# Optimization experiments

Measured on AMD Instinct MI355X. Metric: run time of the kernel, lower is better.

## Reference

```python
import jax, jax.numpy as jnp
import numpy as np

# Mamba-1.4B-like dims
BATCH, SEQ, HID = 1, 2048, 2048
INTER, STATE, DT_RANK, KCONV = 4096, 16, 128, 4


def setup_inputs() -> dict:
    key = jax.random.key(0)
    ks = jax.random.split(key, 8)
    f = jnp.float32
    return {
        "input_states": jax.random.normal(ks[0], (BATCH, SEQ, HID), f),
        "in_proj_w": jax.random.normal(ks[1], (HID, 2 * INTER), f) * (HID ** -0.5),
        "conv_w": jax.random.normal(ks[2], (INTER, 1, KCONV), f) * (KCONV ** -0.5),  # (O, I/groups=1, K) depthwise
        "conv_b": jnp.zeros((INTER,), f),
        "x_proj_w": jax.random.normal(ks[3], (INTER, DT_RANK + 2 * STATE), f) * (INTER ** -0.5),
        "dt_proj_w": jax.random.normal(ks[4], (DT_RANK, INTER), f) * (DT_RANK ** -0.5),
        "dt_proj_b": jax.random.normal(ks[5], (INTER,), f) * 0.1,
        "A_log": jnp.log(jnp.broadcast_to(jnp.arange(1, STATE + 1, dtype=f), (INTER, STATE))),
        "D": jnp.ones((INTER,), f),
        "out_proj_w": jax.random.normal(ks[6], (INTER, HID), f) * (INTER ** -0.5),
    }


def _mamba_forward(input_states, in_proj_w, conv_w, conv_b, x_proj_w,
                   dt_proj_w, dt_proj_b, A_log, D, out_proj_w):
    Bsz, L, _ = input_states.shape
    Idim, _, K = conv_w.shape
    N = A_log.shape[1]
    R = dt_proj_w.shape[0]

    proj = input_states @ in_proj_w                       # (B, L, 2I)
    hidden, gate = jnp.split(proj, 2, axis=-1)            # each (B, L, I)

    # depthwise causal conv over sequence (pad K-1, keep first L outputs)
    xc = jnp.swapaxes(hidden, 1, 2)                       # (B, I, L)
    xc = jax.lax.conv_general_dilated(
        xc, conv_w, window_strides=(1,), padding=((K - 1, K - 1),),
        feature_group_count=Idim)
    xc = xc[:, :, :L] + conv_b[None, :, None]
    u = jax.nn.silu(jnp.swapaxes(xc, 1, 2))               # (B, L, I)

    # input-dependent SSM params
    ssm_in = u @ x_proj_w                                 # (B, L, R + 2N)
    dt_in, Bc, Cc = jnp.split(ssm_in, [R, R + N], axis=-1)
    dt = jax.nn.softplus(dt_in @ dt_proj_w + dt_proj_b)   # (B, L, I)
    A = -jnp.exp(A_log)                                   # (I, N)

    def step(state, xs):
        dt_t, B_t, C_t, u_t = xs                          # (B,I) (B,N) (B,N) (B,I)
        dA = jnp.exp(dt_t[:, :, None] * A[None])          # (B, I, N)
        state = state * dA + (dt_t * u_t)[:, :, None] * B_t[:, None, :]
        y_t = jnp.einsum('bin,bn->bi', state, C_t)
        return state, y_t

    xs = (jnp.swapaxes(dt, 0, 1), jnp.swapaxes(Bc, 0, 1),
          jnp.swapaxes(Cc, 0, 1), jnp.swapaxes(u, 0, 1))
    state0 = jnp.zeros((Bsz, Idim, N), dt.dtype)
    _, ys = jax.lax.scan(step, state0, xs)                # (L, B, I)
    y = jnp.swapaxes(ys, 0, 1)                            # (B, L, I)

    y = (y + u * D) * jax.nn.silu(gate)
    return y @ out_proj_w                                 # (B, L, H)


def reference(input_states, in_proj_w, conv_w, conv_b, x_proj_w,
              dt_proj_w, dt_proj_b, A_log, D, out_proj_w):
    return _mamba_forward(input_states, in_proj_w, conv_w, conv_b, x_proj_w,
                          dt_proj_w, dt_proj_b, A_log, D, out_proj_w)
```

## Files before the change

### kernel.cpp

```cpp
#include <hip/hip_runtime.h>
#include <stdint.h>

#define LSEQ 2048
#define HID  2048
#define IDIM 4096
#define NSTATE 16
#define RRANK 128
#define GDIM 160

#define GCHUNK 64
#define TCHUNK (LSEQ / GCHUNK)

typedef _Float16 f16x8 __attribute__((ext_vector_type(8)));
typedef float f32x4 __attribute__((ext_vector_type(4)));

#define GLOAD_LDS16(g, l) __builtin_amdgcn_global_load_lds( \
    (const __attribute__((address_space(1))) void*)(g),     \
    (__attribute__((address_space(3))) void*)(l), 16, 0, 0)

__global__ void f32_to_f16_kernel(const float* __restrict__ in, _Float16* __restrict__ out, int n) {
    int i = blockIdx.x * 256 + threadIdx.x;
    if (i < n) out[i] = (_Float16)in[i];
}

__global__ __launch_bounds__(256)
void transpose_f32_f16_kernel(const float* __restrict__ in, _Float16* __restrict__ out,
                              int R, int C) {
    __shared__ _Float16 tile[64][66];
    const int c0 = blockIdx.x * 64, r0 = blockIdx.y * 64;
    const int t = threadIdx.x;
    const int tx = t & 15, ty = t >> 4;
    const int ox = t & 7, oy = t >> 3;
    const bool full = (c0 + 64 <= C) && (r0 + 64 <= R);
    if (full) {
        #pragma unroll
        for (int j = 0; j < 4; ++j) {
            int r = ty + j * 16;
            float4 v = *(const float4*)(in + (long)(r0 + r) * C + c0 + tx * 4);
            tile[r][tx * 4 + 0] = (_Float16)v.x;
            tile[r][tx * 4 + 1] = (_Float16)v.y;
            tile[r][tx * 4 + 2] = (_Float16)v.z;
            tile[r][tx * 4 + 3] = (_Float16)v.w;
        }
        __syncthreads();
        #pragma unroll
        for (int j = 0; j < 2; ++j) {
            int c = oy + j * 32;
            f16x8 v;
            #pragma unroll
            for (int e = 0; e < 8; ++e) v[e] = tile[ox * 8 + e][c];
            *(f16x8*)(out + (long)(c0 + c) * R + r0 + ox * 8) = v;
        }
    } else {
        #pragma unroll
        for (int j = 0; j < 4; ++j) {
            int r = ty + j * 16;
            #pragma unroll
            for (int e = 0; e < 4; ++e) {
                int c = c0 + tx * 4 + e;
                float v = (r0 + r < R && c < C) ? in[(long)(r0 + r) * C + c] : 0.f;
                tile[r][tx * 4 + e] = (_Float16)v;
            }
        }
        __syncthreads();
        #pragma unroll
        for (int j = 0; j < 2; ++j) {
            int c = c0 + oy + j * 32;
            if (c < C) {
                #pragma unroll
                for (int e = 0; e < 8; ++e) {
                    int r = r0 + ox * 8 + e;
                    if (r < R) out[(long)c * R + r] = tile[ox * 8 + e][oy + j * 32];
                }
            }
        }
    }
}

#define BM 128
#define BK 64

template <typename CT, int BN_>
__global__ __launch_bounds__(256)
void gemm_bt_kernel(const _Float16* __restrict__ A, const _Float16* __restrict__ Bt,
                    CT* __restrict__ C, int M, int N, int K, int kc) {
    constexpr int NI = BN_ / 32;
    constexpr int NISS_B = BN_ * 8 / 256;
    __shared__ _Float16 As[BM * BK];
    __shared__ _Float16 Bs[BN_ * BK];
    const int m0 = blockIdx.y * BM;
    const int n0 = blockIdx.x * BN_;
    const int t = threadIdx.x;
    const int wave = t >> 6;
    const int lane = t & 63;
    const int wm = wave >> 1, wn = wave & 1;
    const int lrow = lane & 15;
    const int quad = lane >> 4;
    const int sw8 = (lrow & 7) * 8;

    f32x4 acc[4][NI];
    #pragma unroll
    for (int mi = 0; mi < 4; ++mi)
        #pragma unroll
        for (int ni = 0; ni < NI; ++ni)
            #pragma unroll
            for (int r = 0; r < 4; ++r)
                acc[mi][ni][r] = 0.f;

    const int k_begin = blockIdx.z * kc;
    const _Float16* pA[4];
    #pragma unroll
    for (int j = 0; j < 4; ++j) {
        int s = j * 256 + t;
        int row = s >> 3;
        int ch = (s & 7) ^ (row & 7);
        pA[j] = A + (long)(m0 + row) * K + ch * 8 + k_begin;
    }
    const _Float16* pB[NISS_B];
    #pragma unroll
    for (int j = 0; j < NISS_B; ++j) {
        int s = j * 256 + t;
        int row = s >> 3;
        int ch = (s & 7) ^ (row & 7);
        pB[j] = Bt + (long)(n0 + row) * K + ch * 8 + k_begin;
    }

    for (int kk = 0; kk < kc; kk += BK) {
        #pragma unroll
        for (int j = 0; j < 4; ++j) {
            GLOAD_LDS16(pA[j], As + (j * 256 + wave * 64) * 8);
            pA[j] += BK;
        }
        #pragma unroll
        for (int j = 0; j < NISS_B; ++j) {
            GLOAD_LDS16(pB[j], Bs + (j * 256 + wave * 64) * 8);
            pB[j] += BK;
        }
        __syncthreads();

        #pragma unroll
        for (int h = 0; h < 2; ++h) {
            const int qoff = (h * 32 + quad * 8) ^ sw8;
            f16x8 af[4], bf[NI];
            #pragma unroll
            for (int mi = 0; mi < 4; ++mi)
                af[mi] = *(const f16x8*)(As + (wm * 64 + mi * 16 + lrow) * BK + qoff);
            #pragma unroll
            for (int ni = 0; ni < NI; ++ni)
                bf[ni] = *(const f16x8*)(Bs + (wn * (BN_ / 2) + ni * 16 + lrow) * BK + qoff);
            #pragma unroll
            for (int mi = 0; mi < 4; ++mi)
                #pragma unroll
                for (int ni = 0; ni < NI; ++ni)
                    acc[mi][ni] = __builtin_amdgcn_mfma_f32_16x16x32_f16(af[mi], bf[ni], acc[mi][ni], 0, 0, 0);
        }
        __syncthreads();
    }

    CT* Cz = C + (long)blockIdx.z * M * N;
    #pragma unroll
    for (int mi = 0; mi < 4; ++mi) {
        #pragma unroll
        for (int ni = 0; ni < NI; ++ni) {
            int col = n0 + wn * (BN_ / 2) + ni * 16 + lrow;
            if (col < N) {
                #pragma unroll
                for (int r = 0; r < 4; ++r) {
                    int row = m0 + wm * 64 + mi * 16 + quad * 4 + r;
                    Cz[(long)row * N + col] = (CT)acc[mi][ni][r];
                }
            }
        }
    }
}

__global__ void xproj_reduce_kernel(const float* __restrict__ part, float* __restrict__ ssm,
                                    _Float16* __restrict__ dtin) {
    int idx = blockIdx.x * 256 + threadIdx.x;
    if (idx >= LSEQ * GDIM) return;
    int t = idx / GDIM;
    int c = idx - t * GDIM;
    float v = 0.f;
    #pragma unroll
    for (int k = 0; k < 8; ++k)
        v += part[((long)k * LSEQ + t) * 256 + c];
    ssm[idx] = v;
    if (c < RRANK) dtin[t * RRANK + c] = (_Float16)v;
}

__global__ void opart_reduce_kernel(const float* __restrict__ part, float* __restrict__ out) {
    int idx = blockIdx.x * 256 + threadIdx.x;
    out[idx] = part[idx] + part[idx + (long)LSEQ * HID];
}

__global__ void conv_silu_kernel(const _Float16* __restrict__ proj, const float* __restrict__ w,
                                 const float* __restrict__ b, _Float16* __restrict__ u16) {
    int idx = blockIdx.x * 256 + threadIdx.x;
    int i0 = (idx & 511) * 8;
    int t0 = (idx >> 9) * 4;
    f16x8 r[7];
    #pragma unroll
    for (int k = 0; k < 7; ++k) {
        int tt = t0 - 3 + k;
        if (tt >= 0) r[k] = *(const f16x8*)(proj + (long)tt * (2 * IDIM) + i0);
        else         r[k] = f16x8{0,0,0,0,0,0,0,0};
    }
    float4 wv[8]; float bb[8];
    #pragma unroll
    for (int j = 0; j < 8; ++j) { wv[j] = ((const float4*)w)[i0 + j]; bb[j] = b[i0 + j]; }
    #pragma unroll
    for (int tt = 0; tt < 4; ++tt) {
        f16x8 res;
        #pragma unroll
        for (int j = 0; j < 8; ++j) {
            float a = bb[j] + (float)r[tt][j] * wv[j].x + (float)r[tt+1][j] * wv[j].y
                            + (float)r[tt+2][j] * wv[j].z + (float)r[tt+3][j] * wv[j].w;
            res[j] = (_Float16)(a / (1.f + __expf(-a)));
        }
        *(f16x8*)(u16 + (long)(t0 + tt) * IDIM + i0) = res;
    }
}

__device__ __forceinline__ float softplus_f(float x) {
    if (x > 20.f) return x;
    return log1pf(__expf(x));
}
__device__ __forceinline__ float silu_f(float x) {
    return x / (1.f + __expf(-x));
}

__global__ __launch_bounds__(256)
void scan_pass1_kernel(const _Float16* __restrict__ dtlin, const float* __restrict__ dtb,
                       const float* __restrict__ ssm, const _Float16* __restrict__ u16,
                       const float* __restrict__ A_log,
                       float* __restrict__ Pc, float* __restrict__ Sc) {
    const int c = blockIdx.y;
    const int i = blockIdx.x * 256 + threadIdx.x;

    __shared__ float Bs[TCHUNK * 16];
    for (int idx = threadIdx.x; idx < TCHUNK * 16; idx += 256) {
        int t = idx >> 4, n = idx & 15;
        Bs[idx] = ssm[(c * TCHUNK + t) * GDIM + RRANK + n];
    }
    __syncthreads();

    float A[16];
    {
        const float4* Ap = (const float4*)(A_log + i * 16);
        #pragma unroll
        for (int q = 0; q < 4; ++q) {
            float4 v = Ap[q];
            A[q * 4 + 0] = -__expf(v.x);
            A[q * 4 + 1] = -__expf(v.y);
            A[q * 4 + 2] = -__expf(v.z);
            A[q * 4 + 3] = -__expf(v.w);
        }
    }
    const float dtbi = dtb[i];

    float s[16], p[16];
    #pragma unroll
    for (int n = 0; n < 16; ++n) { s[n] = 0.f; p[n] = 1.f; }

    long base = (long)c * TCHUNK * IDIM + i;
    for (int t = 0; t < TCHUNK; ++t) {
        float dt = softplus_f((float)dtlin[base + (long)t * IDIM] + dtbi);
        float dtu = dt * (float)u16[base + (long)t * IDIM];
        #pragma unroll
        for (int n = 0; n < 16; ++n) {
            float dA = __expf(dt * A[n]);
            s[n] = s[n] * dA + dtu * Bs[t * 16 + n];
            p[n] *= dA;
        }
    }

    long o = ((long)c * IDIM + i) * 16;
    #pragma unroll
    for (int q = 0; q < 4; ++q) {
        *(float4*)(Pc + o + q * 4) = make_float4(p[q*4+0], p[q*4+1], p[q*4+2], p[q*4+3]);
        *(float4*)(Sc + o + q * 4) = make_float4(s[q*4+0], s[q*4+1], s[q*4+2], s[q*4+3]);
    }
}

__global__ void scan_combine_kernel(const float* __restrict__ Pc, float* __restrict__ ScInit) {
    int tid = blockIdx.x * 256 + threadIdx.x;
    const long stride = (long)IDIM * 16;
    float p4[4], s4[4];
    #pragma unroll
    for (int k = 0; k < 4; ++k) {
        p4[k] = Pc[(long)k * stride + tid];
        s4[k] = ScInit[(long)k * stride + tid];
    }
    float carry = 0.f;
    for (int g = 0; g < GCHUNK / 4; ++g) {
        float pc[4], sc[4];
        #pragma unroll
        for (int k = 0; k < 4; ++k) { pc[k] = p4[k]; sc[k] = s4[k]; }
        if (g + 1 < GCHUNK / 4) {
            #pragma unroll
            for (int k = 0; k < 4; ++k) {
                long o2 = (long)((g + 1) * 4 + k) * stride + tid;
                p4[k] = Pc[o2];
                s4[k] = ScInit[o2];
            }
        }
        #pragma unroll
        for (int k = 0; k < 4; ++k) {
            long o = (long)(g * 4 + k) * stride + tid;
            ScInit[o] = carry;
            carry = carry * pc[k] + sc[k];
        }
    }
}

__global__ __launch_bounds__(256)
void scan_pass3_kernel(const _Float16* __restrict__ dtlin, const float* __restrict__ dtb,
                       const float* __restrict__ ssm, const _Float16* __restrict__ u16,
                       const _Float16* __restrict__ proj, const float* __restrict__ A_log,
                       const float* __restrict__ Dp, const float* __restrict__ Init,
                       _Float16* __restrict__ y16) {
    const int c = blockIdx.y;
    const int i = blockIdx.x * 256 + threadIdx.x;

    __shared__ float Bs[TCHUNK * 16];
    __shared__ float Cs[TCHUNK * 16];
    for (int idx = threadIdx.x; idx < TCHUNK * 16; idx += 256) {
        int t = idx >> 4, n = idx & 15;
        Bs[idx] = ssm[(c * TCHUNK + t) * GDIM + RRANK + n];
        Cs[idx] = ssm[(c * TCHUNK + t) * GDIM + RRANK + NSTATE + n];
    }
    __syncthreads();

    float A[16];
    {
        const float4* Ap = (const float4*)(A_log + i * 16);
        #pragma unroll
        for (int q = 0; q < 4; ++q) {
            float4 v = Ap[q];
            A[q * 4 + 0] = -__expf(v.x);
            A[q * 4 + 1] = -__expf(v.y);
            A[q * 4 + 2] = -__expf(v.z);
            A[q * 4 + 3] = -__expf(v.w);
        }
    }
    const float dtbi = dtb[i];
    const float Dv = Dp[i];

    float s[16];
    {
        long o = ((long)c * IDIM + i) * 16;
        #pragma unroll
        for (int q = 0; q < 4; ++q) {
            float4 v = *(const float4*)(Init + o + q * 4);
            s[q*4+0] = v.x; s[q*4+1] = v.y; s[q*4+2] = v.z; s[q*4+3] = v.w;
        }
    }

    long base = (long)c * TCHUNK * IDIM + i;
    for (int t = 0; t < TCHUNK; ++t) {
        float dt = softplus_f((float)dtlin[base + (long)t * IDIM] + dtbi);
        float uv = (float)u16[base + (long)t * IDIM];
        float dtu = dt * uv;
        float y = 0.f;
        #pragma unroll
        for (int n = 0; n < 16; ++n) {
            float dA = __expf(dt * A[n]);
            s[n] = s[n] * dA + dtu * Bs[t * 16 + n];
            y += s[n] * Cs[t * 16 + n];
        }
        int tg = c * TCHUNK + t;
        float g = (float)proj[(long)tg * (2 * IDIM) + IDIM + i];
        float out = (y + uv * Dv) * silu_f(g);
        y16[base + (long)t * IDIM] = (_Float16)out;
    }
}

extern "C" void kernel_launch(void* const* d_in, const int* in_sizes, int n_in,
                              void* d_out, int out_size, void* d_ws, size_t ws_size,
                              hipStream_t stream) {
    const float* x_in  = (const float*)d_in[0];
    const float* w_in  = (const float*)d_in[1];
    const float* cw    = (const float*)d_in[2];
    const float* cb    = (const float*)d_in[3];
    const float* xw    = (const float*)d_in[4];
    const float* dtw   = (const float*)d_in[5];
    const float* dtb   = (const float*)d_in[6];
    const float* alog  = (const float*)d_in[7];
    const float* Dp    = (const float*)d_in[8];
    const float* ow    = (const float*)d_in[9];
    float* out = (float*)d_out;

    char* p = (char*)d_ws;
    auto alloc = [&](size_t bytes) { char* r = p; p += (bytes + 255) & ~255ull; return r; };
    _Float16* Xf    = (_Float16*)alloc((size_t)LSEQ * HID * 2);
    _Float16* Wt1   = (_Float16*)alloc((size_t)2 * IDIM * HID * 2);
    _Float16* proj  = (_Float16*)alloc((size_t)LSEQ * 2 * IDIM * 2);
    _Float16* u16   = (_Float16*)alloc((size_t)LSEQ * IDIM * 2);
    _Float16* Wt2   = (_Float16*)alloc((size_t)256 * IDIM * 2);
    float*    ssm   = (float*)alloc((size_t)LSEQ * GDIM * 4);
    _Float16* dtin  = (_Float16*)alloc((size_t)LSEQ * RRANK * 2);
    _Float16* Wt3   = (_Float16*)alloc((size_t)IDIM * RRANK * 2);
    _Float16* dtlin = (_Float16*)alloc((size_t)LSEQ * IDIM * 2);
    _Float16* Wt4   = (_Float16*)alloc((size_t)HID * IDIM * 2);
    _Float16* y16   = (_Float16*)alloc((size_t)LSEQ * IDIM * 2);

    float* xpart = (float*)Wt1;
    float* Pc = (float*)Wt1;
    float* Sc = Pc + (size_t)GCHUNK * IDIM * 16;
    float* opart = (float*)Wt1;

    f32_to_f16_kernel<<<(LSEQ * HID) / 256, 256, 0, stream>>>(x_in, Xf, LSEQ * HID);
    transpose_f32_f16_kernel<<<dim3(2 * IDIM / 64, HID / 64), 256, 0, stream>>>(w_in, Wt1, HID, 2 * IDIM);
    transpose_f32_f16_kernel<<<dim3((GDIM + 63) / 64, IDIM / 64), 256, 0, stream>>>(xw, Wt2, IDIM, GDIM);
    transpose_f32_f16_kernel<<<dim3(IDIM / 64, RRANK / 64), 256, 0, stream>>>(dtw, Wt3, RRANK, IDIM);
    transpose_f32_f16_kernel<<<dim3(HID / 64, IDIM / 64), 256, 0, stream>>>(ow, Wt4, IDIM, HID);

    gemm_bt_kernel<_Float16, 128><<<dim3(2 * IDIM / 128, LSEQ / BM, 1), 256, 0, stream>>>(
        Xf, Wt1, proj, LSEQ, 2 * IDIM, HID, HID);
    conv_silu_kernel<<<(LSEQ / 4) * (IDIM / 8) / 256, 256, 0, stream>>>(proj, cw, cb, u16);
    gemm_bt_kernel<float, 128><<<dim3(2, LSEQ / BM, 8), 256, 0, stream>>>(
        u16, Wt2, xpart, LSEQ, 256, IDIM, IDIM / 8);
    xproj_reduce_kernel<<<(LSEQ * GDIM + 255) / 256, 256, 0, stream>>>(xpart, ssm, dtin);
    gemm_bt_kernel<_Float16, 128><<<dim3(IDIM / 128, LSEQ / BM, 1), 256, 0, stream>>>(
        dtin, Wt3, dtlin, LSEQ, IDIM, RRANK, RRANK);
    scan_pass1_kernel<<<dim3(IDIM / 256, GCHUNK), 256, 0, stream>>>(
        dtlin, dtb, ssm, u16, alog, Pc, Sc);
    scan_combine_kernel<<<(IDIM * NSTATE) / 256, 256, 0, stream>>>(Pc, Sc);
    scan_pass3_kernel<<<dim3(IDIM / 256, GCHUNK), 256, 0, stream>>>(
        dtlin, dtb, ssm, u16, proj, alog, Dp, Sc, y16);
    gemm_bt_kernel<float, 128><<<dim3(HID / 128, LSEQ / BM, 2), 256, 0, stream>>>(
        y16, Wt4, opart, LSEQ, HID, IDIM, IDIM / 2);
    opart_reduce_kernel<<<(LSEQ * HID) / 256, 256, 0, stream>>>(opart, out);
}
```

Measured before the change: 502.1 us.

## Fuse prep kernels, softplus epilogue, fp16 scan carries, two channels per scan thread

Merges the conversion and transpose launches into a single prep kernel. It fuses the dt bias and softplus into the dt-projection GEMM epilogue, so the scan passes read the final dt directly. The scan passes now process two channels per thread with paired fp16 loads, and the chunk carry products and states are stored in fp16 to cut traffic. The output reduction is vectorised with float4. The fp16 carries risk precision loss or underflow, and halving the scan block count may reduce latency hiding.

New measurement: 470.6 us. -6.3%, faster.

```diff
diff --git a/kernel.cpp b/kernel.cpp
--- a/kernel.cpp
+++ b/kernel.cpp
@@ -12,22 +12,26 @@
 #define TCHUNK (LSEQ / GCHUNK)
 
 typedef _Float16 f16x8 __attribute__((ext_vector_type(8)));
+typedef _Float16 f16x2 __attribute__((ext_vector_type(2)));
 typedef float f32x4 __attribute__((ext_vector_type(4)));
 
 #define GLOAD_LDS16(g, l) __builtin_amdgcn_global_load_lds( \
     (const __attribute__((address_space(1))) void*)(g),     \
     (__attribute__((address_space(3))) void*)(l), 16, 0, 0)
 
-__global__ void f32_to_f16_kernel(const float* __restrict__ in, _Float16* __restrict__ out, int n) {
-    int i = blockIdx.x * 256 + threadIdx.x;
-    if (i < n) out[i] = (_Float16)in[i];
-}
-
-__global__ __launch_bounds__(256)
-void transpose_f32_f16_kernel(const float* __restrict__ in, _Float16* __restrict__ out,
-                              int R, int C) {
-    __shared__ _Float16 tile[64][66];
-    const int c0 = blockIdx.x * 64, r0 = blockIdx.y * 64;
+__device__ __forceinline__ float softplus_f(float x) {
+    if (x > 20.f) return x;
+    return log1pf(__expf(x));
+}
+__device__ __forceinline__ float silu_f(float x) {
+    return x / (1.f + __expf(-x));
+}
+
+__device__ __forceinline__ void transpose_tile(const float* __restrict__ in,
+                                               _Float16* __restrict__ out,
+                                               int R, int C, int tr, int tc,
+                                               _Float16 (*tile)[66]) {
+    const int c0 = tc * 64, r0 = tr * 64;
     const int t = threadIdx.x;
     const int tx = t & 15, ty = t >> 4;
     const int ox = t & 7, oy = t >> 3;
@@ -77,13 +81,43 @@
     }
 }
 
+__global__ __launch_bounds__(256)
+void prep_kernel(const float* __restrict__ x_in, const float* __restrict__ w_in,
+                 const float* __restrict__ xw, const float* __restrict__ dtw,
+                 const float* __restrict__ ow,
+                 _Float16* __restrict__ Xf, _Float16* __restrict__ Wt1,
+                 _Float16* __restrict__ Wt2, _Float16* __restrict__ Wt3,
+                 _Float16* __restrict__ Wt4) {
+    __shared__ _Float16 tile[64][66];
+    int b = blockIdx.x;
+    if (b < 4096) { transpose_tile(w_in, Wt1, HID, 2 * IDIM, b / 128, b % 128, tile); return; }
+    b -= 4096;
+    if (b < 192) { transpose_tile(xw, Wt2, IDIM, GDIM, b / 3, b % 3, tile); return; }
+    b -= 192;
+    if (b < 128) { transpose_tile(dtw, Wt3, RRANK, IDIM, b / 64, b % 64, tile); return; }
+    b -= 128;
+    if (b < 2048) { transpose_tile(ow, Wt4, IDIM, HID, b / 32, b % 32, tile); return; }
+    b -= 2048;
+    long base = (long)b * 4096 + threadIdx.x * 16;
+    #pragma unroll
+    for (int h = 0; h < 2; ++h) {
+        float4 a = *(const float4*)(x_in + base + h * 8);
+        float4 c = *(const float4*)(x_in + base + h * 8 + 4);
+        f16x8 v;
+        v[0] = (_Float16)a.x; v[1] = (_Float16)a.y; v[2] = (_Float16)a.z; v[3] = (_Float16)a.w;
+        v[4] = (_Float16)c.x; v[5] = (_Float16)c.y; v[6] = (_Float16)c.z; v[7] = (_Float16)c.w;
+        *(f16x8*)(Xf + base + h * 8) = v;
+    }
+}
+
 #define BM 128
 #define BK 64
 
-template <typename CT, int BN_>
+template <typename CT, int BN_, bool SOFTPLUS>
 __global__ __launch_bounds__(256)
 void gemm_bt_kernel(const _Float16* __restrict__ A, const _Float16* __restrict__ Bt,
-                    CT* __restrict__ C, int M, int N, int K, int kc) {
+                    CT* __restrict__ C, int M, int N, int K, int kc,
+                    const float* __restrict__ bias) {
     constexpr int NI = BN_ / 32;
     constexpr int NISS_B = BN_ * 8 / 256;
     __shared__ _Float16 As[BM * BK];
@@ -164,10 +198,13 @@
         for (int ni = 0; ni < NI; ++ni) {
             int col = n0 + wn * (BN_ / 2) + ni * 16 + lrow;
             if (col < N) {
+                float bv = SOFTPLUS ? bias[col] : 0.f;
                 #pragma unroll
                 for (int r = 0; r < 4; ++r) {
                     int row = m0 + wm * 64 + mi * 16 + quad * 4 + r;
-                    Cz[(long)row * N + col] = (CT)acc[mi][ni][r];
+                    float v = acc[mi][ni][r];
+                    if (SOFTPLUS) v = softplus_f(v + bv);
+                    Cz[(long)row * N + col] = (CT)v;
                 }
             }
         }
@@ -190,7 +227,9 @@
 
 __global__ void opart_reduce_kernel(const float* __restrict__ part, float* __restrict__ out) {
     int idx = blockIdx.x * 256 + threadIdx.x;
-    out[idx] = part[idx] + part[idx + (long)LSEQ * HID];
+    float4 a = ((const float4*)part)[idx];
+    float4 b = ((const float4*)(part + (long)LSEQ * HID))[idx];
+    ((float4*)out)[idx] = make_float4(a.x + b.x, a.y + b.y, a.z + b.z, a.w + b.w);
 }
 
 __global__ void conv_silu_kernel(const _Float16* __restrict__ proj, const float* __restrict__ w,
@@ -221,21 +260,12 @@
     }
 }
 
-__device__ __forceinline__ float softplus_f(float x) {
-    if (x > 20.f) return x;
-    return log1pf(__expf(x));
-}
-__device__ __forceinline__ float silu_f(float x) {
-    return x / (1.f + __expf(-x));
-}
-
 __global__ __launch_bounds__(256)
-void scan_pass1_kernel(const _Float16* __restrict__ dtlin, const float* __restrict__ dtb,
-                       const float* __restrict__ ssm, const _Float16* __restrict__ u16,
-                       const float* __restrict__ A_log,
-                       float* __restrict__ Pc, float* __restrict__ Sc) {
+void scan_pass1_kernel(const _Float16* __restrict__ dtf, const float* __restrict__ ssm,
+                       const _Float16* __restrict__ u16, const float* __restrict__ A_log,
+                       _Float16* __restrict__ Pc, _Float16* __restrict__ Sc) {
     const int c = blockIdx.y;
-    const int i = blockIdx.x * 256 + threadIdx.x;
+    const int i0 = (blockIdx.x * 256 + threadIdx.x) * 2;
 
     __shared__ float Bs[TCHUNK * 16];
     for (int idx = threadIdx.x; idx < TCHUNK * 16; idx += 256) {
@@ -244,83 +274,100 @@
     }
     __syncthreads();
 
-    float A[16];
-    {
-        const float4* Ap = (const float4*)(A_log + i * 16);
+    float A[2][16];
+    #pragma unroll
+    for (int ch = 0; ch < 2; ++ch) {
+        const float4* Ap = (const float4*)(A_log + (long)(i0 + ch) * 16);
         #pragma unroll
         for (int q = 0; q < 4; ++q) {
             float4 v = Ap[q];
-            A[q * 4 + 0] = -__expf(v.x);
-            A[q * 4 + 1] = -__expf(v.y);
-            A[q * 4 + 2] = -__expf(v.z);
-            A[q * 4 + 3] = -__expf(v.w);
-        }
-    }
-    const float dtbi = dtb[i];
-
-    float s[16], p[16];
-    #pragma unroll
-    for (int n = 0; n < 16; ++n) { s[n] = 0.f; p[n] = 1.f; }
-
-    long base = (long)c * TCHUNK * IDIM + i;
+            A[ch][q * 4 + 0] = -__expf(v.x);
+            A[ch][q * 4 + 1] = -__expf(v.y);
+            A[ch][q * 4 + 2] = -__expf(v.z);
+            A[ch][q * 4 + 3] = -__expf(v.w);
+        }
+    }
+
+    float s[2][16], pr[2][16];
+    #pragma unroll
+    for (int ch = 0; ch < 2; ++ch)
+        #pragma unroll
+        for (int n = 0; n < 16; ++n) { s[ch][n] = 0.f; pr[ch][n] = 1.f; }
+
+    long base = (long)c * TCHUNK * IDIM + i0;
     for (int t = 0; t < TCHUNK; ++t) {
-        float dt = softplus_f((float)dtlin[base + (long)t * IDIM] + dtbi);
-        float dtu = dt * (float)u16[base + (long)t * IDIM];
-        #pragma unroll
-        for (int n = 0; n < 16; ++n) {
-            float dA = __expf(dt * A[n]);
-            s[n] = s[n] * dA + dtu * Bs[t * 16 + n];
-            p[n] *= dA;
-        }
-    }
-
-    long o = ((long)c * IDIM + i) * 16;
-    #pragma unroll
-    for (int q = 0; q < 4; ++q) {
-        *(float4*)(Pc + o + q * 4) = make_float4(p[q*4+0], p[q*4+1], p[q*4+2], p[q*4+3]);
-        *(float4*)(Sc + o + q * 4) = make_float4(s[q*4+0], s[q*4+1], s[q*4+2], s[q*4+3]);
-    }
-}
-
-__global__ void scan_combine_kernel(const float* __restrict__ Pc, float* __restrict__ ScInit) {
+        f16x2 dt2 = *(const f16x2*)(dtf + base + (long)t * IDIM);
+        f16x2 u2  = *(const f16x2*)(u16 + base + (long)t * IDIM);
+        #pragma unroll
+        for (int ch = 0; ch < 2; ++ch) {
+            float dt = (float)dt2[ch];
+            float dtu = dt * (float)u2[ch];
+            #pragma unroll
+            for (int n = 0; n < 16; ++n) {
+                float dA = __expf(dt * A[ch][n]);
+                s[ch][n] = s[ch][n] * dA + dtu * Bs[t * 16 + n];
+                pr[ch][n] *= dA;
+            }
+        }
+    }
+
+    long o = ((long)c * IDIM + i0) * 16;
+    #pragma unroll
+    for (int ch = 0; ch < 2; ++ch) {
+        #pragma unroll
+        for (int q = 0; q < 2; ++q) {
+            f16x8 pv, sv;
+            #pragma unroll
+            for (int e = 0; e < 8; ++e) {
+                pv[e] = (_Float16)pr[ch][q * 8 + e];
+                sv[e] = (_Float16)s[ch][q * 8 + e];
+            }
+            *(f16x8*)(Pc + o + ch * 16 + q * 8) = pv;
+            *(f16x8*)(Sc + o + ch * 16 + q * 8) = sv;
+        }
+    }
+}
+
+__global__ void scan_combine_kernel(const _Float16* __restrict__ Pc, _Float16* __restrict__ ScInit) {
     int tid = blockIdx.x * 256 + threadIdx.x;
     const long stride = (long)IDIM * 16;
-    float p4[4], s4[4];
+    const long off = (long)tid * 2;
+    f16x2 p4[4], s4[4];
     #pragma unroll
     for (int k = 0; k < 4; ++k) {
-        p4[k] = Pc[(long)k * stride + tid];
-        s4[k] = ScInit[(long)k * stride + tid];
-    }
-    float carry = 0.f;
+        p4[k] = *(const f16x2*)(Pc + (long)k * stride + off);
+        s4[k] = *(const f16x2*)(ScInit + (long)k * stride + off);
+    }
+    float c0 = 0.f, c1 = 0.f;
     for (int g = 0; g < GCHUNK / 4; ++g) {
-        float pc[4], sc[4];
+        f16x2 pc[4], sc[4];
         #pragma unroll
         for (int k = 0; k < 4; ++k) { pc[k] = p4[k]; sc[k] = s4[k]; }
         if (g + 1 < GCHUNK / 4) {
             #pragma unroll
             for (int k = 0; k < 4; ++k) {
-                long o2 = (long)((g + 1) * 4 + k) * stride + tid;
-                p4[k] = Pc[o2];
-                s4[k] = ScInit[o2];
+                long o2 = (long)((g + 1) * 4 + k) * stride + off;
+                p4[k] = *(const f16x2*)(Pc + o2);
+                s4[k] = *(const f16x2*)(ScInit + o2);
             }
         }
         #pragma unroll
         for (int k = 0; k < 4; ++k) {
-            long o = (long)(g * 4 + k) * stride + tid;
-            ScInit[o] = carry;
-            carry = carry * pc[k] + sc[k];
+            long o = (long)(g * 4 + k) * stride + off;
+            *(f16x2*)(ScInit + o) = f16x2{(_Float16)c0, (_Float16)c1};
+            c0 = c0 * (float)pc[k][0] + (float)sc[k][0];
+            c1 = c1 * (float)pc[k][1] + (float)sc[k][1];
         }
     }
 }
 
 __global__ __launch_bounds__(256)
-void scan_pass3_kernel(const _Float16* __restrict__ dtlin, const float* __restrict__ dtb,
-                       const float* __restrict__ ssm, const _Float16* __restrict__ u16,
-                       const _Float16* __restrict__ proj, const float* __restrict__ A_log,
-                       const float* __restrict__ Dp, const float* __restrict__ Init,
-                       _Float16* __restrict__ y16) {
+void scan_pass3_kernel(const _Float16* __restrict__ dtf, const float* __restrict__ ssm,
+                       const _Float16* __restrict__ u16, const _Float16* __restrict__ proj,
+                       const float* __restrict__ A_log, const float* __restrict__ Dp,
+                       const _Float16* __restrict__ Init, _Float16* __restrict__ y16) {
     const int c = blockIdx.y;
-    const int i = blockIdx.x * 256 + threadIdx.x;
+    const int i0 = (blockIdx.x * 256 + threadIdx.x) * 2;
 
     __shared__ float Bs[TCHUNK * 16];
     __shared__ float Cs[TCHUNK * 16];
@@ -331,47 +378,58 @@
     }
     __syncthreads();
 
-    float A[16];
-    {
-        const float4* Ap = (const float4*)(A_log + i * 16);
+    float A[2][16];
+    #pragma unroll
+    for (int ch = 0; ch < 2; ++ch) {
+        const float4* Ap = (const float4*)(A_log + (long)(i0 + ch) * 16);
         #pragma unroll
         for (int q = 0; q < 4; ++q) {
             float4 v = Ap[q];
-            A[q * 4 + 0] = -__expf(v.x);
-            A[q * 4 + 1] = -__expf(v.y);
-            A[q * 4 + 2] = -__expf(v.z);
-            A[q * 4 + 3] = -__expf(v.w);
-        }
-    }
-    const float dtbi = dtb[i];
-    const float Dv = Dp[i];
-
-    float s[16];
+            A[ch][q * 4 + 0] = -__expf(v.x);
+            A[ch][q * 4 + 1] = -__expf(v.y);
+            A[ch][q * 4 + 2] = -__expf(v.z);
+            A[ch][q * 4 + 3] = -__expf(v.w);
+        }
+    }
+    float2 Dv = *(const float2*)(Dp + i0);
+
+    float s[2][16];
     {
-        long o = ((long)c * IDIM + i) * 16;
-        #pragma unroll
-        for (int q = 0; q < 4; ++q) {
-            float4 v = *(const float4*)(Init + o + q * 4);
-            s[q*4+0] = v.x; s[q*4+1] = v.y; s[q*4+2] = v.z; s[q*4+3] = v.w;
-        }
-    }
-
-    long base = (long)c * TCHUNK * IDIM + i;
+        long o = ((long)c * IDIM + i0) * 16;
+        #pragma unroll
+        for (int ch = 0; ch < 2; ++ch)
+            #pragma unroll
+            for (int q = 0; q < 2; ++q) {
+                f16x8 v = *(const f16x8*)(Init + o + ch * 16 + q * 8);
+                #pragma unroll
+                for (int e = 0; e < 8; ++e) s[ch][q * 8 + e] = (float)v[e];
+            }
+    }
+
+    long base = (long)c * TCHUNK * IDIM + i0;
     for (int t = 0; t < TCHUNK; ++t) {
-        float dt = softplus_f((float)dtlin[base + (long)t * IDIM] + dtbi);
-        float uv = (float)u16[base + (long)t * IDIM];
-        float dtu = dt * uv;
-        float y = 0.f;
-        #pragma unroll
-        for (int n = 0; n < 16; ++n) {
-            float dA = __expf(dt * A[n]);
-            s[n] = s[n] * dA + dtu * Bs[t * 16 + n];
-            y += s[n] * Cs[t * 16 + n];
-        }
+        f16x2 dt2 = *(const f16x2*)(dtf + base + (long)t * IDIM);
+        f16x2 u2  = *(const f16x2*)(u16 + base + (long)t * IDIM);
         int tg = c * TCHUNK + t;
-        float g = (float)proj[(long)tg * (2 * IDIM) + IDIM + i];
-        float out = (y + uv * Dv) * silu_f(g);
-        y16[base + (long)t * IDIM] = (_Float16)out;
+        f16x2 g2 = *(const f16x2*)(proj + (long)tg * (2 * IDIM) + IDIM + i0);
+        f16x2 res;
+        #pragma unroll
+        for (int ch = 0; ch < 2; ++ch) {
+            float dt = (float)dt2[ch];
+            float uv = (float)u2[ch];
+            float dtu = dt * uv;
+            float y = 0.f;
+            #pragma unroll
+            for (int n = 0; n < 16; ++n) {
+                float dA = __expf(dt * A[ch][n]);
+                s[ch][n] = s[ch][n] * dA + dtu * Bs[t * 16 + n];
+                y += s[ch][n] * Cs[t * 16 + n];
+            }
+            float g = (float)g2[ch];
+            float Dch = ch ? Dv.y : Dv.x;
+            res[ch] = (_Float16)((y + uv * Dch) * silu_f(g));
+        }
+        *(f16x2*)(y16 + base + (long)t * IDIM) = res;
     }
 }
 
@@ -400,35 +458,30 @@
     float*    ssm   = (float*)alloc((size_t)LSEQ * GDIM * 4);
     _Float16* dtin  = (_Float16*)alloc((size_t)LSEQ * RRANK * 2);
     _Float16* Wt3   = (_Float16*)alloc((size_t)IDIM * RRANK * 2);
-    _Float16* dtlin = (_Float16*)alloc((size_t)LSEQ * IDIM * 2);
+    _Float16* dtf   = (_Float16*)alloc((size_t)LSEQ * IDIM * 2);
     _Float16* Wt4   = (_Float16*)alloc((size_t)HID * IDIM * 2);
     _Float16* y16   = (_Float16*)alloc((size_t)LSEQ * IDIM * 2);
 
     float* xpart = (float*)Wt1;
-    float* Pc = (float*)Wt1;
-    float* Sc = Pc + (size_t)GCHUNK * IDIM * 16;
+    _Float16* Pc = (_Float16*)Wt1;
+    _Float16* Sc = Pc + (size_t)GCHUNK * IDIM * 16;
     float* opart = (float*)Wt1;
 
-    f32_to_f16_kernel<<<(LSEQ * HID) / 256, 256, 0, stream>>>(x_in, Xf, LSEQ * HID);
-    transpose_f32_f16_kernel<<<dim3(2 * IDIM / 64, HID / 64), 256, 0, stream>>>(w_in, Wt1, HID, 2 * IDIM);
-    transpose_f32_f16_kernel<<<dim3((GDIM + 63) / 64, IDIM / 64), 256, 0, stream>>>(xw, Wt2, IDIM, GDIM);
-    transpose_f32_f16_kernel<<<dim3(IDIM / 64, RRANK / 64), 256, 0, stream>>>(dtw, Wt3, RRANK, IDIM);
-    transpose_f32_f16_kernel<<<dim3(HID / 64, IDIM / 64), 256, 0, stream>>>(ow, Wt4, IDIM, HID);
-
-    gemm_bt_kernel<_Float16, 128><<<dim3(2 * IDIM / 128, LSEQ / BM, 1), 256, 0, stream>>>(
-        Xf, Wt1, proj, LSEQ, 2 * IDIM, HID, HID);
+    prep_kernel<<<7488, 256, 0, stream>>>(x_in, w_in, xw, dtw, ow, Xf, Wt1, Wt2, Wt3, Wt4);
+    gemm_bt_kernel<_Float16, 128, false><<<dim3(2 * IDIM / 128, LSEQ / BM, 1), 256, 0, stream>>>(
+        Xf, Wt1, proj, LSEQ, 2 * IDIM, HID, HID, nullptr);
     conv_silu_kernel<<<(LSEQ / 4) * (IDIM / 8) / 256, 256, 0, stream>>>(proj, cw, cb, u16);
-    gemm_bt_kernel<float, 128><<<dim3(2, LSEQ / BM, 8), 256, 0, stream>>>(
-        u16, Wt2, xpart, LSEQ, 256, IDIM, IDIM / 8);
+    gemm_bt_kernel<float, 128, false><<<dim3(2, LSEQ / BM, 8), 256, 0, stream>>>(
+        u16, Wt2, xpart, LSEQ, 256, IDIM, IDIM / 8, nullptr);
     xproj_reduce_kernel<<<(LSEQ * GDIM + 255) / 256, 256, 0, stream>>>(xpart, ssm, dtin);
-    gemm_bt_kernel<_Float16, 128><<<dim3(IDIM / 128, LSEQ / BM, 1), 256, 0, stream>>>(
-        dtin, Wt3, dtlin, LSEQ, IDIM, RRANK, RRANK);
-    scan_pass1_kernel<<<dim3(IDIM / 256, GCHUNK), 256, 0, stream>>>(
-        dtlin, dtb, ssm, u16, alog, Pc, Sc);
-    scan_combine_kernel<<<(IDIM * NSTATE) / 256, 256, 0, stream>>>(Pc, Sc);
-    scan_pass3_kernel<<<dim3(IDIM / 256, GCHUNK), 256, 0, stream>>>(
-        dtlin, dtb, ssm, u16, proj, alog, Dp, Sc, y16);
-    gemm_bt_kernel<float, 128><<<dim3(HID / 128, LSEQ / BM, 2), 256, 0, stream>>>(
-        y16, Wt4, opart, LSEQ, HID, IDIM, IDIM / 2);
-    opart_reduce_kernel<<<(LSEQ * HID) / 256, 256, 0, stream>>>(opart, out);
-}
+    gemm_bt_kernel<_Float16, 128, true><<<dim3(IDIM / 128, LSEQ / BM, 1), 256, 0, stream>>>(
+        dtin, Wt3, dtf, LSEQ, IDIM, RRANK, RRANK, dtb);
+    scan_pass1_kernel<<<dim3(IDIM / 512, GCHUNK), 256, 0, stream>>>(
+        dtf, ssm, u16, alog, Pc, Sc);
+    scan_combine_kernel<<<(IDIM * NSTATE / 2) / 256, 256, 0, stream>>>(Pc, Sc);
+    scan_pass3_kernel<<<dim3(IDIM / 512, GCHUNK), 256, 0, stream>>>(
+        dtf, ssm, u16, proj, alog, Dp, Sc, y16);
+    gemm_bt_kernel<float, 128, false><<<dim3(HID / 128, LSEQ / BM, 2), 256, 0, stream>>>(
+        y16, Wt4, opart, LSEQ, HID, IDIM, IDIM / 2, nullptr);
+    opart_reduce_kernel<<<(LSEQ * HID / 4) / 256, 256, 0, stream>>>(opart, out);
+}
```
